# Kernel optimization log

Hardware: AMD Instinct MI355X
Metric: run time of the kernel (lower is better)

The kernel has to match this reference:

```python
import jax, jax.numpy as jnp
import numpy as np

D_MODEL = 1024
BATCH, SEQ = 4, 4096


def setup_inputs() -> dict:
    key = jax.random.key(0)
    ks = jax.random.split(key, 4)
    scale = 1.0 / np.sqrt(D_MODEL)  # lecun_normal-ish init for Dense kernels
    x = jax.random.normal(ks[0], (BATCH, SEQ, D_MODEL), dtype=jnp.float32)
    Wf = jax.random.normal(ks[1], (D_MODEL, D_MODEL), dtype=jnp.float32) * scale
    Wi = jax.random.normal(ks[2], (D_MODEL, D_MODEL), dtype=jnp.float32) * scale
    Wb = jax.random.normal(ks[3], (D_MODEL, D_MODEL), dtype=jnp.float32) * scale
    bf = jnp.full((D_MODEL,), -4.0, dtype=jnp.float32)  # forget bias -> f~0.018
    bi = jnp.full((D_MODEL,), 4.0, dtype=jnp.float32)   # input bias  -> i~0.982
    bb = jnp.zeros((D_MODEL,), dtype=jnp.float32)
    return {"x": x, "Wf": Wf, "bf": bf, "Wi": Wi, "bi": bi, "Wb": Wb, "bb": bb}


def _scan_combine(c1, c2):
    a1, b1 = c1
    a2, b2 = c2
    # linear recurrence composition: h = a2*(a1*h_prev + b1) + b2
    return a1 * a2, a2 * b1 + b2


def reference(x, Wf, bf, Wi, bi, Wb, bb):
    # gates + drive: [B, S, D]
    f = jax.nn.sigmoid(jnp.einsum('bsd,de->bse', x, Wf) + bf)
    i = jax.nn.sigmoid(jnp.einsum('bsd,de->bse', x, Wi) + bi)
    b = (jnp.einsum('bsd,de->bse', x, Wb) + bb) / jnp.sqrt(jnp.float32(x.shape[-1]))
    a = (1.0 - f).astype(jnp.complex64)
    b_gated = (i * b).astype(jnp.complex64)
    # parallel associative scan over time axis: h_t = a_t * h_{t-1} + b_t
    _, state = jax.lax.associative_scan(_scan_combine, (a, b_gated), axis=1)
    return state.real
```

## Files before the change

### kernel.cpp

```cpp
#include <hip/hip_runtime.h>
#include <cstdint>

#define D_MODEL 1024
#define BATCH 4
#define SEQ 4096
#define M_TOT (BATCH*SEQ)

#define BM 128
#define BN 128
#define BK 64
#define NKT (D_MODEL/BK)

#define XS_BYTES 16384
#define WG_BYTES 16384
#define TILE_BYTES (XS_BYTES + 3*WG_BYTES)
#define SMEM_BYTES (2*TILE_BYTES)

#define NCHUNK 64
#define CHUNK 64

typedef __bf16 bf16x8 __attribute__((ext_vector_type(8)));
typedef float f32x4 __attribute__((ext_vector_type(4)));
typedef unsigned short u16x8 __attribute__((ext_vector_type(8)));

static __device__ __forceinline__ unsigned short f2bf(float f) {
    unsigned int u = __float_as_uint(f);
    return (unsigned short)((u + 0x7fffu + ((u >> 16) & 1u)) >> 16);
}
static __device__ __forceinline__ float ubf(unsigned short u) {
    return __uint_as_float((unsigned int)u << 16);
}

__global__ void k_convert_x(const float* __restrict__ x, unsigned short* __restrict__ xb) {
    int i = blockIdx.x * 256 + threadIdx.x;
    const float4* p = (const float4*)x;
    float4 v0 = p[2*i], v1 = p[2*i+1];
    u16x8 r;
    r[0] = f2bf(v0.x); r[1] = f2bf(v0.y); r[2] = f2bf(v0.z); r[3] = f2bf(v0.w);
    r[4] = f2bf(v1.x); r[5] = f2bf(v1.y); r[6] = f2bf(v1.z); r[7] = f2bf(v1.w);
    *(u16x8*)(xb + (size_t)i * 8) = r;
}

__global__ void k_transpose_w(const float* __restrict__ Wf, const float* __restrict__ Wi,
                              const float* __restrict__ Wb, unsigned short* __restrict__ wt) {
    __shared__ float tile[32][33];
    int g = blockIdx.z;
    const float* W = (g == 0) ? Wf : (g == 1) ? Wi : Wb;
    int n0 = blockIdx.x * 32, k0 = blockIdx.y * 32;
    int tx = threadIdx.x, ty = threadIdx.y;
    for (int j = 0; j < 4; ++j)
        tile[ty + j*8][tx] = W[(size_t)(k0 + ty + j*8) * D_MODEL + n0 + tx];
    __syncthreads();
    for (int j = 0; j < 4; ++j) {
        int n = n0 + ty + j*8;
        wt[(size_t)g * D_MODEL * D_MODEL + (size_t)n * D_MODEL + k0 + tx] = f2bf(tile[tx][ty + j*8]);
    }
}

#define GL16(gp, lp) \
    __builtin_amdgcn_global_load_lds((const __attribute__((address_space(1))) void*)(gp), \
                                     (__attribute__((address_space(3))) void*)(lp), 16, 0, 0)

__launch_bounds__(512, 2)
__global__ void k_gemm_gates(const unsigned short* __restrict__ xb, const unsigned short* __restrict__ wt,
                             const float* __restrict__ bfv, const float* __restrict__ biv,
                             const float* __restrict__ bbv,
                             unsigned short* __restrict__ f_out, unsigned short* __restrict__ bg_out,
                             float* __restrict__ Ac, float* __restrict__ Bc) {
    extern __shared__ char smem[];
    const int tid  = threadIdx.x;
    const int wave = tid >> 6;
    const int lane = tid & 63;
    const int lr = lane & 15, lg = lane >> 4;
    const int m0 = blockIdx.x * BM;
    const int n0 = blockIdx.y * BN;
    const int wr = wave >> 2;
    const int wrow = wr * 64;
    const int wcol = (wave & 3) * 32;

    const int srow = tid >> 3;
    const int scb  = ((tid & 7) * 16) ^ ((srow & 7) << 4);
    const unsigned short* s0 = xb + (size_t)(m0 + srow)      * D_MODEL + (scb >> 1);
    const unsigned short* s1 = xb + (size_t)(m0 + 64 + srow) * D_MODEL + (scb >> 1);
    const unsigned short* s2 = wt + 0ull*D_MODEL*D_MODEL + (size_t)(n0 + srow)      * D_MODEL + (scb >> 1);
    const unsigned short* s3 = wt + 0ull*D_MODEL*D_MODEL + (size_t)(n0 + 64 + srow) * D_MODEL + (scb >> 1);
    const unsigned short* s4 = wt + 1ull*D_MODEL*D_MODEL + (size_t)(n0 + srow)      * D_MODEL + (scb >> 1);
    const unsigned short* s5 = wt + 1ull*D_MODEL*D_MODEL + (size_t)(n0 + 64 + srow) * D_MODEL + (scb >> 1);
    const unsigned short* s6 = wt + 2ull*D_MODEL*D_MODEL + (size_t)(n0 + srow)      * D_MODEL + (scb >> 1);
    const unsigned short* s7 = wt + 2ull*D_MODEL*D_MODEL + (size_t)(n0 + 64 + srow) * D_MODEL + (scb >> 1);

#define STAGE(bufsel) do { \
        char* _b = smem + (bufsel)*TILE_BYTES + wave*1024; \
        GL16(s0, _b + 0*8192); GL16(s1, _b + 1*8192); \
        GL16(s2, _b + 2*8192); GL16(s3, _b + 3*8192); \
        GL16(s4, _b + 4*8192); GL16(s5, _b + 5*8192); \
        GL16(s6, _b + 6*8192); GL16(s7, _b + 7*8192); \
        s0 += BK; s1 += BK; s2 += BK; s3 += BK; \
        s4 += BK; s5 += BK; s6 += BK; s7 += BK; \
    } while (0)

    f32x4 acc[3][4][2] = {};
    const int sxor = (lr & 7) << 4;

    STAGE(0);
    __syncthreads();

    for (int kt = 0; kt < NKT; ++kt) {
        if (kt + 1 < NKT) STAGE((kt + 1) & 1);

        const char* tb = smem + (kt & 1) * TILE_BYTES;
        #pragma unroll
        for (int kk = 0; kk < 2; ++kk) {
            const int ko = (kk*64 + lg*16) ^ sxor;
            bf16x8 af[2];
            bf16x8 bw[3][2];
            #pragma unroll
            for (int mi = 0; mi < 2; ++mi)
                af[mi] = *(const bf16x8*)(tb + (wrow + mi*16 + lr)*128 + ko);
            #pragma unroll
            for (int g = 0; g < 3; ++g)
                #pragma unroll
                for (int ni = 0; ni < 2; ++ni)
                    bw[g][ni] = *(const bf16x8*)(tb + XS_BYTES + g*WG_BYTES +
                                                 (wcol + ni*16 + lr)*128 + ko);
            #pragma unroll
            for (int g = 0; g < 3; ++g)
                #pragma unroll
                for (int mi = 0; mi < 2; ++mi)
                    #pragma unroll
                    for (int ni = 0; ni < 2; ++ni)
                        acc[g][mi][ni] = __builtin_amdgcn_mfma_f32_16x16x32_bf16(
                            af[mi], bw[g][ni], acc[g][mi][ni], 0, 0, 0);
            bf16x8 af2[2];
            #pragma unroll
            for (int mi = 0; mi < 2; ++mi)
                af2[mi] = *(const bf16x8*)(tb + (wrow + (mi+2)*16 + lr)*128 + ko);
            #pragma unroll
            for (int g = 0; g < 3; ++g)
                #pragma unroll
                for (int mi = 0; mi < 2; ++mi)
                    #pragma unroll
                    for (int ni = 0; ni < 2; ++ni)
                        acc[g][mi+2][ni] = __builtin_amdgcn_mfma_f32_16x16x32_bf16(
                            af2[mi], bw[g][ni], acc[g][mi+2][ni], 0, 0, 0);
        }
        __syncthreads();
    }

    #pragma unroll
    for (int ni = 0; ni < 2; ++ni) {
        const int col = n0 + wcol + ni*16 + lr;
        const float vbf = bfv[col], vbi = biv[col], vbb = bbv[col];
        float qA[4], qB[4];
        #pragma unroll
        for (int mi = 0; mi < 4; ++mi) {
            float Ap = 1.0f, Bp = 0.0f;
            #pragma unroll
            for (int r = 0; r < 4; ++r) {
                const int row = m0 + wrow + mi*16 + lg*4 + r;
                const float zf = acc[0][mi][ni][r] + vbf;
                const float zi = acc[1][mi][ni][r] + vbi;
                const float zb = (acc[2][mi][ni][r] + vbb) * 0.03125f;
                const float fg = 1.0f / (1.0f + __expf(-zf));
                const float ig = 1.0f / (1.0f + __expf(-zi));
                const unsigned short fu  = f2bf(fg);
                const unsigned short bgu = f2bf(ig * zb);
                const float a_r  = 1.0f - ubf(fu);
                const float bg_r = ubf(bgu);
                const size_t o = (size_t)row * D_MODEL + col;
                f_out[o]  = fu;
                bg_out[o] = bgu;
                Bp = fmaf(a_r, Bp, bg_r);
                Ap *= a_r;
            }
            qA[mi] = Ap; qB[mi] = Bp;
        }
        float CA = 1.0f, CB = 0.0f;
        #pragma unroll
        for (int q = 0; q < 4; ++q) {
            float A = qA[q], B = qB[q];
            float Ao = __shfl_xor(A, 16), Bo = __shfl_xor(B, 16);
            float B1 = (lg & 1) ? fmaf(A, Bo, B) : fmaf(Ao, B, Bo);
            float A1 = A * Ao;
            Ao = __shfl_xor(A1, 32); Bo = __shfl_xor(B1, 32);
            float B2 = (lg & 2) ? fmaf(A1, Bo, B1) : fmaf(Ao, B1, Bo);
            float A2 = A1 * Ao;
            CB = fmaf(A2, CB, B2);
            CA = CA * A2;
        }
        if (lg == 0) {
            const int chG = blockIdx.x * 2 + wr;
            Ac[(size_t)chG * D_MODEL + col] = CA;
            Bc[(size_t)chG * D_MODEL + col] = CB;
        }
    }
#undef STAGE
}

__global__ void k_chunk_prefix(const float* __restrict__ Ac, const float* __restrict__ Bc,
                               float* __restrict__ H) {
    const int d = (blockIdx.x & 3) * 256 + threadIdx.x;
    const int b = blockIdx.x >> 2;
    float h = 0.0f;
    for (int c = 0; c < NCHUNK; ++c) {
        const size_t o = ((size_t)b * NCHUNK + c) * D_MODEL + d;
        H[o] = h;
        h = fmaf(Ac[o], h, Bc[o]);
    }
}

__global__ void k_apply(const unsigned short* __restrict__ f, const unsigned short* __restrict__ bg,
                        const float* __restrict__ H, float* __restrict__ out) {
    const int d0 = (blockIdx.x & 1) * 512 + threadIdx.x * 2;
    const int c = (blockIdx.x >> 1) & 63;
    const int b = blockIdx.x >> 7;
    const size_t base = ((size_t)b * SEQ + (size_t)c * CHUNK) * D_MODEL + d0;
    const size_t hoff = ((size_t)b * NCHUNK + c) * D_MODEL + d0;
    float h0 = H[hoff], h1 = H[hoff + 1];
    for (int t = 0; t < CHUNK; ++t) {
        const size_t o = base + (size_t)t * D_MODEL;
        const unsigned int fv = *(const unsigned int*)(f + o);
        const unsigned int gv = *(const unsigned int*)(bg + o);
        const float a0 = 1.0f - __uint_as_float(fv << 16);
        const float a1 = 1.0f - __uint_as_float(fv & 0xffff0000u);
        const float b0 = __uint_as_float(gv << 16);
        const float b1 = __uint_as_float(gv & 0xffff0000u);
        h0 = fmaf(a0, h0, b0);
        h1 = fmaf(a1, h1, b1);
        *(float2*)(out + o) = make_float2(h0, h1);
    }
}

extern "C" void kernel_launch(void* const* d_in, const int* in_sizes, int n_in,
                              void* d_out, int out_size, void* d_ws, size_t ws_size,
                              hipStream_t stream) {
    const float* x   = (const float*)d_in[0];
    const float* Wf  = (const float*)d_in[1];
    const float* bfv = (const float*)d_in[2];
    const float* Wi  = (const float*)d_in[3];
    const float* biv = (const float*)d_in[4];
    const float* Wb  = (const float*)d_in[5];
    const float* bbv = (const float*)d_in[6];
    float* out = (float*)d_out;

    char* ws = (char*)d_ws;
    unsigned short* fbuf  = (unsigned short*)ws;
    unsigned short* bgbuf = (unsigned short*)(ws + (32ull << 20));
    unsigned short* xb    = (unsigned short*)(ws + (64ull << 20));
    unsigned short* wt    = (unsigned short*)(ws + (96ull << 20));
    float* Ac = (float*)(ws + (102ull << 20));
    float* Bc = (float*)(ws + (103ull << 20));
    float* Hb = (float*)(ws + (64ull << 20));

    hipFuncSetAttribute((const void*)k_gemm_gates,
                        hipFuncAttributeMaxDynamicSharedMemorySize, SMEM_BYTES);

    hipLaunchKernelGGL(k_convert_x, dim3((M_TOT * D_MODEL / 8) / 256), dim3(256), 0, stream, x, xb);
    hipLaunchKernelGGL(k_transpose_w, dim3(32, 32, 3), dim3(32, 8), 0, stream, Wf, Wi, Wb, wt);
    hipLaunchKernelGGL(k_gemm_gates, dim3(M_TOT / BM, D_MODEL / BN), dim3(512), SMEM_BYTES, stream,
                       xb, wt, bfv, biv, bbv, fbuf, bgbuf, Ac, Bc);
    hipLaunchKernelGGL(k_chunk_prefix, dim3(BATCH * (D_MODEL / 256)), dim3(256), 0, stream,
                       Ac, Bc, Hb);
    hipLaunchKernelGGL(k_apply, dim3(BATCH * NCHUNK * 2), dim3(256), 0, stream,
                       fbuf, bgbuf, Hb, out);
}
```

Baseline: 163.7 us.

## Retile gates GEMM to 256x64 with phased load/MFMA pipeline and XCD swizzle

```diff
diff --git a/kernel.cpp b/kernel.cpp
--- a/kernel.cpp
+++ b/kernel.cpp
@@ -6,13 +6,13 @@
 #define SEQ 4096
 #define M_TOT (BATCH*SEQ)
 
-#define BM 128
-#define BN 128
+#define BM 256
+#define BNG 64
 #define BK 64
 #define NKT (D_MODEL/BK)
 
-#define XS_BYTES 16384
-#define WG_BYTES 16384
+#define XS_BYTES (BM*BK*2)
+#define WG_BYTES (BNG*BK*2)
 #define TILE_BYTES (XS_BYTES + 3*WG_BYTES)
 #define SMEM_BYTES (2*TILE_BYTES)
 
@@ -61,7 +61,7 @@
     __builtin_amdgcn_global_load_lds((const __attribute__((address_space(1))) void*)(gp), \
                                      (__attribute__((address_space(3))) void*)(lp), 16, 0, 0)
 
-__launch_bounds__(512, 2)
+__launch_bounds__(512)
 __global__ void k_gemm_gates(const unsigned short* __restrict__ xb, const unsigned short* __restrict__ wt,
                              const float* __restrict__ bfv, const float* __restrict__ biv,
                              const float* __restrict__ bbv,
@@ -72,95 +72,129 @@
     const int wave = tid >> 6;
     const int lane = tid & 63;
     const int lr = lane & 15, lg = lane >> 4;
-    const int m0 = blockIdx.x * BM;
-    const int n0 = blockIdx.y * BN;
+    const int bid = blockIdx.x;
+    const int swz = (bid & 7) * 128 + (bid >> 3);
+    const int mb = swz >> 4;
+    const int nb = swz & 15;
+    const int m0 = mb * BM;
+    const int n0 = nb * BNG;
     const int wr = wave >> 2;
-    const int wrow = wr * 64;
-    const int wcol = (wave & 3) * 32;
+    const int wc = wave & 3;
+    const int wrow = wr * 128;
 
     const int srow = tid >> 3;
     const int scb  = ((tid & 7) * 16) ^ ((srow & 7) << 4);
-    const unsigned short* s0 = xb + (size_t)(m0 + srow)      * D_MODEL + (scb >> 1);
-    const unsigned short* s1 = xb + (size_t)(m0 + 64 + srow) * D_MODEL + (scb >> 1);
-    const unsigned short* s2 = wt + 0ull*D_MODEL*D_MODEL + (size_t)(n0 + srow)      * D_MODEL + (scb >> 1);
-    const unsigned short* s3 = wt + 0ull*D_MODEL*D_MODEL + (size_t)(n0 + 64 + srow) * D_MODEL + (scb >> 1);
-    const unsigned short* s4 = wt + 1ull*D_MODEL*D_MODEL + (size_t)(n0 + srow)      * D_MODEL + (scb >> 1);
-    const unsigned short* s5 = wt + 1ull*D_MODEL*D_MODEL + (size_t)(n0 + 64 + srow) * D_MODEL + (scb >> 1);
-    const unsigned short* s6 = wt + 2ull*D_MODEL*D_MODEL + (size_t)(n0 + srow)      * D_MODEL + (scb >> 1);
-    const unsigned short* s7 = wt + 2ull*D_MODEL*D_MODEL + (size_t)(n0 + 64 + srow) * D_MODEL + (scb >> 1);
-
-#define STAGE(bufsel) do { \
-        char* _b = smem + (bufsel)*TILE_BYTES + wave*1024; \
-        GL16(s0, _b + 0*8192); GL16(s1, _b + 1*8192); \
-        GL16(s2, _b + 2*8192); GL16(s3, _b + 3*8192); \
-        GL16(s4, _b + 4*8192); GL16(s5, _b + 5*8192); \
-        GL16(s6, _b + 6*8192); GL16(s7, _b + 7*8192); \
-        s0 += BK; s1 += BK; s2 += BK; s3 += BK; \
-        s4 += BK; s5 += BK; s6 += BK; s7 += BK; \
-    } while (0)
-
-    f32x4 acc[3][4][2] = {};
+    const unsigned short* sA0 = xb + (size_t)(m0 +   0 + srow) * D_MODEL + (scb >> 1);
+    const unsigned short* sA1 = xb + (size_t)(m0 +  64 + srow) * D_MODEL + (scb >> 1);
+    const unsigned short* sA2 = xb + (size_t)(m0 + 128 + srow) * D_MODEL + (scb >> 1);
+    const unsigned short* sA3 = xb + (size_t)(m0 + 192 + srow) * D_MODEL + (scb >> 1);
+    const unsigned short* sB0 = wt + 0ull*D_MODEL*D_MODEL + (size_t)(n0 + srow) * D_MODEL + (scb >> 1);
+    const unsigned short* sB1 = wt + 1ull*D_MODEL*D_MODEL + (size_t)(n0 + srow) * D_MODEL + (scb >> 1);
+    const unsigned short* sB2 = wt + 2ull*D_MODEL*D_MODEL + (size_t)(n0 + srow) * D_MODEL + (scb >> 1);
+
+#define STAGE_A(db) do { char* _d = smem + (db)*TILE_BYTES + wave*1024; \
+        GL16(sA0, _d + 0*8192); GL16(sA1, _d + 1*8192); \
+        GL16(sA2, _d + 2*8192); GL16(sA3, _d + 3*8192); \
+        sA0 += BK; sA1 += BK; sA2 += BK; sA3 += BK; } while (0)
+#define STAGE_B01(db) do { char* _d = smem + (db)*TILE_BYTES + XS_BYTES + wave*1024; \
+        GL16(sB0, _d + 0*8192); GL16(sB1, _d + 1*8192); \
+        sB0 += BK; sB1 += BK; } while (0)
+#define STAGE_B2(db) do { char* _d = smem + (db)*TILE_BYTES + XS_BYTES + 2*8192 + wave*1024; \
+        GL16(sB2, _d); sB2 += BK; } while (0)
+
+    f32x4 acc[3][8] = {};
     const int sxor = (lr & 7) << 4;
 
-    STAGE(0);
-    __syncthreads();
-
-    for (int kt = 0; kt < NKT; ++kt) {
-        if (kt + 1 < NKT) STAGE((kt + 1) & 1);
-
+    STAGE_A(0); STAGE_B01(0); STAGE_B2(0);
+    asm volatile("s_waitcnt vmcnt(1)" ::: "memory");
+    __builtin_amdgcn_s_barrier();
+
+    bf16x8 af[2][4], af2[2][4], bw01[2][2], bw2[2];
+
+#define READS_P1(tb) do { _Pragma("unroll") for (int kk = 0; kk < 2; ++kk) { \
+        const int ko = (kk*64 + lg*16) ^ sxor; \
+        _Pragma("unroll") for (int mi = 0; mi < 4; ++mi) \
+            af[kk][mi] = *(const bf16x8*)((tb) + (wrow + mi*16 + lr)*128 + ko); \
+        _Pragma("unroll") for (int g = 0; g < 2; ++g) \
+            bw01[kk][g] = *(const bf16x8*)((tb) + XS_BYTES + g*WG_BYTES + (wc*16 + lr)*128 + ko); } } while (0)
+#define READS_P2(tb) do { _Pragma("unroll") for (int kk = 0; kk < 2; ++kk) { \
+        const int ko = (kk*64 + lg*16) ^ sxor; \
+        _Pragma("unroll") for (int mi = 0; mi < 4; ++mi) \
+            af2[kk][mi] = *(const bf16x8*)((tb) + (wrow + (mi+4)*16 + lr)*128 + ko); } } while (0)
+#define READS_P3(tb) do { _Pragma("unroll") for (int kk = 0; kk < 2; ++kk) { \
+        const int ko = (kk*64 + lg*16) ^ sxor; \
+        bw2[kk] = *(const bf16x8*)((tb) + XS_BYTES + 2*WG_BYTES + (wc*16 + lr)*128 + ko); } } while (0)
+#define MFMA_P1 do { _Pragma("unroll") for (int g = 0; g < 2; ++g) \
+        _Pragma("unroll") for (int mi = 0; mi < 4; ++mi) \
+        _Pragma("unroll") for (int kk = 0; kk < 2; ++kk) \
+            acc[g][mi] = __builtin_amdgcn_mfma_f32_16x16x32_bf16(af[kk][mi], bw01[kk][g], acc[g][mi], 0,0,0); } while (0)
+#define MFMA_P2 do { _Pragma("unroll") for (int g = 0; g < 2; ++g) \
+        _Pragma("unroll") for (int mi = 0; mi < 4; ++mi) \
+        _Pragma("unroll") for (int kk = 0; kk < 2; ++kk) \
+            acc[g][mi+4] = __builtin_amdgcn_mfma_f32_16x16x32_bf16(af2[kk][mi], bw01[kk][g], acc[g][mi+4], 0,0,0); } while (0)
+#define MFMA_P3 do { _Pragma("unroll") for (int mi = 0; mi < 4; ++mi) \
+        _Pragma("unroll") for (int kk = 0; kk < 2; ++kk) { \
+            acc[2][mi]   = __builtin_amdgcn_mfma_f32_16x16x32_bf16(af[kk][mi],  bw2[kk], acc[2][mi],   0,0,0); \
+            acc[2][mi+4] = __builtin_amdgcn_mfma_f32_16x16x32_bf16(af2[kk][mi], bw2[kk], acc[2][mi+4], 0,0,0); } } while (0)
+#define LGKM_FENCE do { asm volatile("s_waitcnt lgkmcnt(0)" ::: "memory"); \
+        __builtin_amdgcn_sched_barrier(0); } while (0)
+
+    #pragma unroll 1
+    for (int kt = 0; kt < NKT - 1; ++kt) {
         const char* tb = smem + (kt & 1) * TILE_BYTES;
+        const int db = (kt + 1) & 1;
+        READS_P1(tb);
+        STAGE_A(db);
+        __builtin_amdgcn_s_barrier();
+        LGKM_FENCE;
+        __builtin_amdgcn_s_setprio(1); MFMA_P1; __builtin_amdgcn_s_setprio(0);
+        __builtin_amdgcn_s_barrier();
+        READS_P2(tb);
+        STAGE_B01(db);
+        asm volatile("s_waitcnt vmcnt(6)" ::: "memory");
+        __builtin_amdgcn_s_barrier();
+        LGKM_FENCE;
+        __builtin_amdgcn_s_setprio(1); MFMA_P2; __builtin_amdgcn_s_setprio(0);
+        __builtin_amdgcn_s_barrier();
+        READS_P3(tb);
+        STAGE_B2(db);
+        asm volatile("s_waitcnt vmcnt(1)" ::: "memory");
+        __builtin_amdgcn_s_barrier();
+        LGKM_FENCE;
+        __builtin_amdgcn_s_setprio(1); MFMA_P3; __builtin_amdgcn_s_setprio(0);
+        __builtin_amdgcn_s_barrier();
+    }
+    {
+        const char* tb = smem + ((NKT - 1) & 1) * TILE_BYTES;
+        READS_P1(tb);
+        __builtin_amdgcn_s_barrier();
+        LGKM_FENCE;
+        __builtin_amdgcn_s_setprio(1); MFMA_P1; __builtin_amdgcn_s_setprio(0);
+        __builtin_amdgcn_s_barrier();
+        READS_P2(tb);
+        asm volatile("s_waitcnt vmcnt(0)" ::: "memory");
+        __builtin_amdgcn_s_barrier();
+        LGKM_FENCE;
+        __builtin_amdgcn_s_setprio(1); MFMA_P2; __builtin_amdgcn_s_setprio(0);
+        __builtin_amdgcn_s_barrier();
+        READS_P3(tb);
+        LGKM_FENCE;
+        __builtin_amdgcn_s_setprio(1); MFMA_P3; __builtin_amdgcn_s_setprio(0);
+    }
+
+    {
+        const int col = n0 + wc*16 + lr;
+        const float vbf = bfv[col], vbi = biv[col], vbb = bbv[col];
+        float sA[2][4], sB[2][4];
         #pragma unroll
-        for (int kk = 0; kk < 2; ++kk) {
-            const int ko = (kk*64 + lg*16) ^ sxor;
-            bf16x8 af[2];
-            bf16x8 bw[3][2];
-            #pragma unroll
-            for (int mi = 0; mi < 2; ++mi)
-                af[mi] = *(const bf16x8*)(tb + (wrow + mi*16 + lr)*128 + ko);
-            #pragma unroll
-            for (int g = 0; g < 3; ++g)
-                #pragma unroll
-                for (int ni = 0; ni < 2; ++ni)
-                    bw[g][ni] = *(const bf16x8*)(tb + XS_BYTES + g*WG_BYTES +
-                                                 (wcol + ni*16 + lr)*128 + ko);
-            #pragma unroll
-            for (int g = 0; g < 3; ++g)
-                #pragma unroll
-                for (int mi = 0; mi < 2; ++mi)
-                    #pragma unroll
-                    for (int ni = 0; ni < 2; ++ni)
-                        acc[g][mi][ni] = __builtin_amdgcn_mfma_f32_16x16x32_bf16(
-                            af[mi], bw[g][ni], acc[g][mi][ni], 0, 0, 0);
-            bf16x8 af2[2];
-            #pragma unroll
-            for (int mi = 0; mi < 2; ++mi)
-                af2[mi] = *(const bf16x8*)(tb + (wrow + (mi+2)*16 + lr)*128 + ko);
-            #pragma unroll
-            for (int g = 0; g < 3; ++g)
-                #pragma unroll
-                for (int mi = 0; mi < 2; ++mi)
-                    #pragma unroll
-                    for (int ni = 0; ni < 2; ++ni)
-                        acc[g][mi+2][ni] = __builtin_amdgcn_mfma_f32_16x16x32_bf16(
-                            af2[mi], bw[g][ni], acc[g][mi+2][ni], 0, 0, 0);
-        }
-        __syncthreads();
-    }
-
-    #pragma unroll
-    for (int ni = 0; ni < 2; ++ni) {
-        const int col = n0 + wcol + ni*16 + lr;
-        const float vbf = bfv[col], vbi = biv[col], vbb = bbv[col];
-        float qA[4], qB[4];
-        #pragma unroll
-        for (int mi = 0; mi < 4; ++mi) {
+        for (int mi = 0; mi < 8; ++mi) {
             float Ap = 1.0f, Bp = 0.0f;
             #pragma unroll
             for (int r = 0; r < 4; ++r) {
                 const int row = m0 + wrow + mi*16 + lg*4 + r;
-                const float zf = acc[0][mi][ni][r] + vbf;
-                const float zi = acc[1][mi][ni][r] + vbi;
-                const float zb = (acc[2][mi][ni][r] + vbb) * 0.03125f;
+                const float zf = acc[0][mi][r] + vbf;
+                const float zi = acc[1][mi][r] + vbi;
+                const float zb = (acc[2][mi][r] + vbb) * 0.03125f;
                 const float fg = 1.0f / (1.0f + __expf(-zf));
                 const float ig = 1.0f / (1.0f + __expf(-zi));
                 const unsigned short fu  = f2bf(fg);
@@ -173,28 +207,31 @@
                 Bp = fmaf(a_r, Bp, bg_r);
                 Ap *= a_r;
             }
-            qA[mi] = Ap; qB[mi] = Bp;
+            sA[mi >> 2][mi & 3] = Ap;
+            sB[mi >> 2][mi & 3] = Bp;
         }
-        float CA = 1.0f, CB = 0.0f;
         #pragma unroll
-        for (int q = 0; q < 4; ++q) {
-            float A = qA[q], B = qB[q];
-            float Ao = __shfl_xor(A, 16), Bo = __shfl_xor(B, 16);
-            float B1 = (lg & 1) ? fmaf(A, Bo, B) : fmaf(Ao, B, Bo);
-            float A1 = A * Ao;
-            Ao = __shfl_xor(A1, 32); Bo = __shfl_xor(B1, 32);
-            float B2 = (lg & 2) ? fmaf(A1, Bo, B1) : fmaf(Ao, B1, Bo);
-            float A2 = A1 * Ao;
-            CB = fmaf(A2, CB, B2);
-            CA = CA * A2;
+        for (int half = 0; half < 2; ++half) {
+            float CA = 1.0f, CB = 0.0f;
+            #pragma unroll
+            for (int q = 0; q < 4; ++q) {
+                float A = sA[half][q], B = sB[half][q];
+                float Ao = __shfl_xor(A, 16), Bo = __shfl_xor(B, 16);
+                float B1 = (lg & 1) ? fmaf(A, Bo, B) : fmaf(Ao, B, Bo);
+                float A1 = A * Ao;
+                Ao = __shfl_xor(A1, 32); Bo = __shfl_xor(B1, 32);
+                float B2 = (lg & 2) ? fmaf(A1, Bo, B1) : fmaf(Ao, B1, Bo);
+                float A2 = A1 * Ao;
+                CB = fmaf(A2, CB, B2);
+                CA = CA * A2;
+            }
+            if (lg == 0) {
+                const int chG = mb * 4 + wr * 2 + half;
+                Ac[(size_t)chG * D_MODEL + col] = CA;
+                Bc[(size_t)chG * D_MODEL + col] = CB;
+            }
         }
-        if (lg == 0) {
-            const int chG = blockIdx.x * 2 + wr;
-            Ac[(size_t)chG * D_MODEL + col] = CA;
-            Bc[(size_t)chG * D_MODEL + col] = CB;
-        }
-    }
-#undef STAGE
+    }
 }
 
 __global__ void k_chunk_prefix(const float* __restrict__ Ac, const float* __restrict__ Bc,
@@ -257,7 +294,7 @@
 
     hipLaunchKernelGGL(k_convert_x, dim3((M_TOT * D_MODEL / 8) / 256), dim3(256), 0, stream, x, xb);
     hipLaunchKernelGGL(k_transpose_w, dim3(32, 32, 3), dim3(32, 8), 0, stream, Wf, Wi, Wb, wt);
-    hipLaunchKernelGGL(k_gemm_gates, dim3(M_TOT / BM, D_MODEL / BN), dim3(512), SMEM_BYTES, stream,
+    hipLaunchKernelGGL(k_gemm_gates, dim3((M_TOT / BM) * (D_MODEL / BNG)), dim3(512), SMEM_BYTES, stream,
                        xb, wt, bfv, biv, bbv, fbuf, bgbuf, Ac, Bc);
     hipLaunchKernelGGL(k_chunk_prefix, dim3(BATCH * (D_MODEL / 256)), dim3(256), 0, stream,
                        Ac, Bc, Hb);
```

Measured after the change: 168.4 us. +2.9%, slower.

## Shrink GEMM N-tile to 64 with 256-thread blocks, swizzle grid, interleave f/bg output

Applied to the files above, without the earlier changes.

```diff
diff --git a/kernel.cpp b/kernel.cpp
--- a/kernel.cpp
+++ b/kernel.cpp
@@ -7,12 +7,12 @@
 #define M_TOT (BATCH*SEQ)
 
 #define BM 128
-#define BN 128
+#define BNG 64
 #define BK 64
 #define NKT (D_MODEL/BK)
 
-#define XS_BYTES 16384
-#define WG_BYTES 16384
+#define XS_BYTES (BM*BK*2)
+#define WG_BYTES (BNG*BK*2)
 #define TILE_BYTES (XS_BYTES + 3*WG_BYTES)
 #define SMEM_BYTES (2*TILE_BYTES)
 
@@ -61,42 +61,49 @@
     __builtin_amdgcn_global_load_lds((const __attribute__((address_space(1))) void*)(gp), \
                                      (__attribute__((address_space(3))) void*)(lp), 16, 0, 0)
 
-__launch_bounds__(512, 2)
+__launch_bounds__(256, 2)
 __global__ void k_gemm_gates(const unsigned short* __restrict__ xb, const unsigned short* __restrict__ wt,
                              const float* __restrict__ bfv, const float* __restrict__ biv,
                              const float* __restrict__ bbv,
-                             unsigned short* __restrict__ f_out, unsigned short* __restrict__ bg_out,
+                             unsigned int* __restrict__ fbg_out,
                              float* __restrict__ Ac, float* __restrict__ Bc) {
     extern __shared__ char smem[];
     const int tid  = threadIdx.x;
     const int wave = tid >> 6;
     const int lane = tid & 63;
     const int lr = lane & 15, lg = lane >> 4;
-    const int m0 = blockIdx.x * BM;
-    const int n0 = blockIdx.y * BN;
-    const int wr = wave >> 2;
+    const int bid = blockIdx.x;
+    const int swz = (bid & 7) * 256 + (bid >> 3);
+    const int mb = swz >> 4;
+    const int nb = swz & 15;
+    const int m0 = mb * BM;
+    const int n0 = nb * BNG;
+    const int wr = wave >> 1;
+    const int wc = wave & 1;
     const int wrow = wr * 64;
-    const int wcol = (wave & 3) * 32;
-
-    const int srow = tid >> 3;
-    const int scb  = ((tid & 7) * 16) ^ ((srow & 7) << 4);
-    const unsigned short* s0 = xb + (size_t)(m0 + srow)      * D_MODEL + (scb >> 1);
-    const unsigned short* s1 = xb + (size_t)(m0 + 64 + srow) * D_MODEL + (scb >> 1);
-    const unsigned short* s2 = wt + 0ull*D_MODEL*D_MODEL + (size_t)(n0 + srow)      * D_MODEL + (scb >> 1);
-    const unsigned short* s3 = wt + 0ull*D_MODEL*D_MODEL + (size_t)(n0 + 64 + srow) * D_MODEL + (scb >> 1);
-    const unsigned short* s4 = wt + 1ull*D_MODEL*D_MODEL + (size_t)(n0 + srow)      * D_MODEL + (scb >> 1);
-    const unsigned short* s5 = wt + 1ull*D_MODEL*D_MODEL + (size_t)(n0 + 64 + srow) * D_MODEL + (scb >> 1);
-    const unsigned short* s6 = wt + 2ull*D_MODEL*D_MODEL + (size_t)(n0 + srow)      * D_MODEL + (scb >> 1);
-    const unsigned short* s7 = wt + 2ull*D_MODEL*D_MODEL + (size_t)(n0 + 64 + srow) * D_MODEL + (scb >> 1);
-
-#define STAGE(bufsel) do { \
-        char* _b = smem + (bufsel)*TILE_BYTES + wave*1024; \
-        GL16(s0, _b + 0*8192); GL16(s1, _b + 1*8192); \
-        GL16(s2, _b + 2*8192); GL16(s3, _b + 3*8192); \
-        GL16(s4, _b + 4*8192); GL16(s5, _b + 5*8192); \
-        GL16(s6, _b + 6*8192); GL16(s7, _b + 7*8192); \
-        s0 += BK; s1 += BK; s2 += BK; s3 += BK; \
-        s4 += BK; s5 += BK; s6 += BK; s7 += BK; \
+    const int wcol = wc * 32;
+
+    const int srl = tid >> 3;
+    const int scb = ((tid & 7) * 16) ^ ((srl & 7) << 4);
+    const unsigned short* sA  = xb + (size_t)(m0 + srl) * D_MODEL + (scb >> 1);
+    const unsigned short* sB0 = wt + 0ull*D_MODEL*D_MODEL + (size_t)(n0 + srl) * D_MODEL + (scb >> 1);
+    const unsigned short* sB1 = wt + 1ull*D_MODEL*D_MODEL + (size_t)(n0 + srl) * D_MODEL + (scb >> 1);
+    const unsigned short* sB2 = wt + 2ull*D_MODEL*D_MODEL + (size_t)(n0 + srl) * D_MODEL + (scb >> 1);
+
+#define STAGE(db) do { \
+        char* _d = smem + (db)*TILE_BYTES + wave*1024; \
+        GL16(sA + 0*32*D_MODEL, _d + 0*4096); \
+        GL16(sA + 1*32*D_MODEL, _d + 1*4096); \
+        GL16(sA + 2*32*D_MODEL, _d + 2*4096); \
+        GL16(sA + 3*32*D_MODEL, _d + 3*4096); \
+        char* _e = _d + XS_BYTES; \
+        GL16(sB0,                _e + 0*4096); \
+        GL16(sB0 + 32*D_MODEL,   _e + 1*4096); \
+        GL16(sB1,                _e + 2*4096); \
+        GL16(sB1 + 32*D_MODEL,   _e + 3*4096); \
+        GL16(sB2,                _e + 4*4096); \
+        GL16(sB2 + 32*D_MODEL,   _e + 5*4096); \
+        sA += BK; sB0 += BK; sB1 += BK; sB2 += BK; \
     } while (0)
 
     f32x4 acc[3][4][2] = {};
@@ -107,42 +114,29 @@
 
     for (int kt = 0; kt < NKT; ++kt) {
         if (kt + 1 < NKT) STAGE((kt + 1) & 1);
-
         const char* tb = smem + (kt & 1) * TILE_BYTES;
         #pragma unroll
         for (int kk = 0; kk < 2; ++kk) {
             const int ko = (kk*64 + lg*16) ^ sxor;
-            bf16x8 af[2];
             bf16x8 bw[3][2];
-            #pragma unroll
-            for (int mi = 0; mi < 2; ++mi)
-                af[mi] = *(const bf16x8*)(tb + (wrow + mi*16 + lr)*128 + ko);
             #pragma unroll
             for (int g = 0; g < 3; ++g)
                 #pragma unroll
                 for (int ni = 0; ni < 2; ++ni)
                     bw[g][ni] = *(const bf16x8*)(tb + XS_BYTES + g*WG_BYTES +
                                                  (wcol + ni*16 + lr)*128 + ko);
+            bf16x8 af[4];
+            #pragma unroll
+            for (int mi = 0; mi < 4; ++mi)
+                af[mi] = *(const bf16x8*)(tb + (wrow + mi*16 + lr)*128 + ko);
             #pragma unroll
             for (int g = 0; g < 3; ++g)
                 #pragma unroll
-                for (int mi = 0; mi < 2; ++mi)
+                for (int mi = 0; mi < 4; ++mi)
                     #pragma unroll
                     for (int ni = 0; ni < 2; ++ni)
                         acc[g][mi][ni] = __builtin_amdgcn_mfma_f32_16x16x32_bf16(
                             af[mi], bw[g][ni], acc[g][mi][ni], 0, 0, 0);
-            bf16x8 af2[2];
-            #pragma unroll
-            for (int mi = 0; mi < 2; ++mi)
-                af2[mi] = *(const bf16x8*)(tb + (wrow + (mi+2)*16 + lr)*128 + ko);
-            #pragma unroll
-            for (int g = 0; g < 3; ++g)
-                #pragma unroll
-                for (int mi = 0; mi < 2; ++mi)
-                    #pragma unroll
-                    for (int ni = 0; ni < 2; ++ni)
-                        acc[g][mi+2][ni] = __builtin_amdgcn_mfma_f32_16x16x32_bf16(
-                            af2[mi], bw[g][ni], acc[g][mi+2][ni], 0, 0, 0);
         }
         __syncthreads();
     }
@@ -167,9 +161,8 @@
                 const unsigned short bgu = f2bf(ig * zb);
                 const float a_r  = 1.0f - ubf(fu);
                 const float bg_r = ubf(bgu);
-                const size_t o = (size_t)row * D_MODEL + col;
-                f_out[o]  = fu;
-                bg_out[o] = bgu;
+                fbg_out[(size_t)row * D_MODEL + col] =
+                    (unsigned int)fu | ((unsigned int)bgu << 16);
                 Bp = fmaf(a_r, Bp, bg_r);
                 Ap *= a_r;
             }
@@ -189,7 +182,7 @@
             CA = CA * A2;
         }
         if (lg == 0) {
-            const int chG = blockIdx.x * 2 + wr;
+            const int chG = mb * 2 + wr;
             Ac[(size_t)chG * D_MODEL + col] = CA;
             Bc[(size_t)chG * D_MODEL + col] = CB;
         }
@@ -209,7 +202,7 @@
     }
 }
 
-__global__ void k_apply(const unsigned short* __restrict__ f, const unsigned short* __restrict__ bg,
+__global__ void k_apply(const unsigned int* __restrict__ fbg,
                         const float* __restrict__ H, float* __restrict__ out) {
     const int d0 = (blockIdx.x & 1) * 512 + threadIdx.x * 2;
     const int c = (blockIdx.x >> 1) & 63;
@@ -219,12 +212,11 @@
     float h0 = H[hoff], h1 = H[hoff + 1];
     for (int t = 0; t < CHUNK; ++t) {
         const size_t o = base + (size_t)t * D_MODEL;
-        const unsigned int fv = *(const unsigned int*)(f + o);
-        const unsigned int gv = *(const unsigned int*)(bg + o);
-        const float a0 = 1.0f - __uint_as_float(fv << 16);
-        const float a1 = 1.0f - __uint_as_float(fv & 0xffff0000u);
-        const float b0 = __uint_as_float(gv << 16);
-        const float b1 = __uint_as_float(gv & 0xffff0000u);
+        const uint2 v = *(const uint2*)(fbg + o);
+        const float a0 = 1.0f - __uint_as_float(v.x << 16);
+        const float b0 = __uint_as_float(v.x & 0xffff0000u);
+        const float a1 = 1.0f - __uint_as_float(v.y << 16);
+        const float b1 = __uint_as_float(v.y & 0xffff0000u);
         h0 = fmaf(a0, h0, b0);
         h1 = fmaf(a1, h1, b1);
         *(float2*)(out + o) = make_float2(h0, h1);
@@ -244,8 +236,7 @@
     float* out = (float*)d_out;
 
     char* ws = (char*)d_ws;
-    unsigned short* fbuf  = (unsigned short*)ws;
-    unsigned short* bgbuf = (unsigned short*)(ws + (32ull << 20));
+    unsigned int*   fbg   = (unsigned int*)ws;
     unsigned short* xb    = (unsigned short*)(ws + (64ull << 20));
     unsigned short* wt    = (unsigned short*)(ws + (96ull << 20));
     float* Ac = (float*)(ws + (102ull << 20));
@@ -257,10 +248,10 @@
 
     hipLaunchKernelGGL(k_convert_x, dim3((M_TOT * D_MODEL / 8) / 256), dim3(256), 0, stream, x, xb);
     hipLaunchKernelGGL(k_transpose_w, dim3(32, 32, 3), dim3(32, 8), 0, stream, Wf, Wi, Wb, wt);
-    hipLaunchKernelGGL(k_gemm_gates, dim3(M_TOT / BM, D_MODEL / BN), dim3(512), SMEM_BYTES, stream,
-                       xb, wt, bfv, biv, bbv, fbuf, bgbuf, Ac, Bc);
+    hipLaunchKernelGGL(k_gemm_gates, dim3((M_TOT / BM) * (D_MODEL / BNG)), dim3(256), SMEM_BYTES, stream,
+                       xb, wt, bfv, biv, bbv, fbg, Ac, Bc);
     hipLaunchKernelGGL(k_chunk_prefix, dim3(BATCH * (D_MODEL / 256)), dim3(256), 0, stream,
                        Ac, Bc, Hb);
     hipLaunchKernelGGL(k_apply, dim3(BATCH * NCHUNK * 2), dim3(256), 0, stream,
-                       fbuf, bgbuf, Hb, out);
-}
+                       fbg, Hb, out);
+}
```

After: 167.5 us. +2.3%, slower.
